# Kernel optimization log

Hardware: AMD Instinct MI355X
Metric: run time of the kernel (lower is better)

The kernel has to match this reference:

```python
import jax, jax.numpy as jnp
import numpy as np
from jax import lax

# Dense emulation of the irregular graph stage (repo helpers img2graph /
# IrregularMaxPool2d / GraphConv2d): nodes = pixels of the stride-4 grid.
# Where pooling_mask==1, a 2x2 block is max-pooled (pooled value replicated
# over the block) and subsequent GraphConv2d gathers neighbors with offset 2
# (dilation 2); where mask==0 the node keeps resolution and offset 1.


def _conv(x, w, b, dil=1):
    p = dil  # SAME padding for a 3x3 kernel with dilation `dil`
    y = lax.conv_general_dilated(x, w, (1, 1), ((p, p), (p, p)),
                                 rhs_dilation=(dil, dil),
                                 dimension_numbers=('NCHW', 'OIHW', 'NCHW'))
    return y + b[None, :, None, None]


def _maxpool2(x):
    return lax.reduce_window(x, -jnp.inf, lax.max, (1, 1, 2, 2), (1, 1, 2, 2), 'VALID')


def _up2(x):
    return jnp.repeat(jnp.repeat(x, 2, axis=2), 2, axis=3)


def setup_inputs() -> dict:
    key = jax.random.key(0)
    ks = jax.random.split(key, 12)
    B, H, W = 4, 384, 384
    inp = {
        'batch': jax.random.normal(ks[0], (B, 3, H, W), jnp.float32),
        'pooling_mask': jax.random.randint(ks[1], (B, 1, H // 8, W // 8), 0, 2, jnp.int32),
    }
    cfg = [(3, 64), (64, 64), (64, 128), (128, 128), (128, 256),
           (256, 256), (256, 256), (256, 512), (512, 512), (512, 512)]
    for i, (cin, cout) in enumerate(cfg):
        scale = float(np.sqrt(2.0 / (cin * 9)))  # He init for 3x3 conv
        inp[f'W{i+1}'] = jax.random.normal(ks[2 + (i % 10)], (cout, cin, 3, 3), jnp.float32) * scale
        inp[f'b{i+1}'] = jnp.zeros((cout,), jnp.float32)
    return inp


def reference(batch, pooling_mask, W1, b1, W2, b2, W3, b3, W4, b4, W5, b5,
              W6, b6, W7, b7, W8, b8, W9, b9, W10, b10):
    x = jax.nn.relu(_conv(batch, W1, b1))
    x = jax.nn.relu(_conv(x, W2, b2))
    x = _maxpool2(x)                                  # H/2
    x = jax.nn.relu(_conv(x, W3, b3))
    x = jax.nn.relu(_conv(x, W4, b4))
    x = _maxpool2(x)                                  # H/4 (OS4)
    x = jax.nn.relu(_conv(x, W5, b5))
    x = jax.nn.relu(_conv(x, W6, b6))
    x = jax.nn.relu(_conv(x, W7, b7))
    # img2graph + IrregularMaxPool2d (number_pools=1)
    m = (pooling_mask > 0).astype(x.dtype)            # [B,1,H/8,W/8]
    m_up = _up2(m)                                    # [B,1,H/4,W/4]
    x = m_up * _up2(_maxpool2(x)) + (1.0 - m_up) * x  # pool 2x2 where mask==1

    # GraphConv2d: per-node neighbor offset = 1 + mask (spatially varying dilation)
    def gconv(h, w, b):
        return m_up * _conv(h, w, b, dil=2) + (1.0 - m_up) * _conv(h, w, b, dil=1)

    x = jax.nn.relu(gconv(x, W8, b8))
    x = jax.nn.relu(gconv(x, W9, b9))
    x = jax.nn.relu(gconv(x, W10, b10))               # use_relu=True
    return x  # graph2img: nodes already laid out on the stride-4 grid
```

## Files before the change

### kernel.cpp

```cpp
#include <hip/hip_runtime.h>


typedef __attribute__((ext_vector_type(8))) short short8;
typedef __attribute__((ext_vector_type(4))) float f32x4;

__device__ __forceinline__ float b2f(ushort u) {
    return __uint_as_float(((unsigned)u) << 16);
}
__device__ __forceinline__ ushort f2b(float f) {
    unsigned x = __float_as_uint(f);
    x += 0x7FFFu + ((x >> 16) & 1u);
    return (ushort)(x >> 16);
}
__device__ __forceinline__ ushort bmax(ushort a, ushort b) {
    return b2f(a) > b2f(b) ? a : b;
}

__global__ __launch_bounds__(256)
void repack_w(const float* __restrict__ w, ushort* __restrict__ wp, int Cin, int Cout)
{
    int n = Cout * Cin * 9;
    int i = blockIdx.x * 256 + threadIdx.x;
    if (i >= n) return;
    int CBl = Cin / 32;
    int c   = i & 31;
    int co  = (i >> 5) % Cout;
    int cbt = i / (32 * Cout);
    int cb  = cbt % CBl;
    int t   = cbt / CBl;
    int ci  = cb * 32 + c;
    wp[i] = f2b(w[((size_t)co * Cin + ci) * 9 + t]);
}

__global__ __launch_bounds__(256)
void l1_conv(const float* __restrict__ in, const float* __restrict__ w,
             const float* __restrict__ bias, ushort* __restrict__ out)
{
    const int H = 384, W = 384;
    __shared__ float s[3][18][18];
    const int tid = threadIdx.x;
    const int tilesX = W / 16;
    const int x0 = (blockIdx.x % tilesX) * 16;
    const int y0 = (blockIdx.x / tilesX) * 16;
    const int b  = blockIdx.z;

    for (int i = tid; i < 3 * 18 * 18; i += 256) {
        int ci = i / (18 * 18);
        int r  = i % (18 * 18);
        int iy = r / 18, ix = r % 18;
        int gy = y0 - 1 + iy, gx = x0 - 1 + ix;
        float v = 0.f;
        if ((unsigned)gy < (unsigned)H && (unsigned)gx < (unsigned)W)
            v = in[((size_t)(b * 3 + ci) * H + gy) * W + gx];
        s[ci][iy][ix] = v;
    }
    __syncthreads();

    const int tx = tid & 15, ty = tid >> 4;
    float iv[3][3][3];
    #pragma unroll
    for (int ci = 0; ci < 3; ++ci)
        #pragma unroll
        for (int ky = 0; ky < 3; ++ky)
            #pragma unroll
            for (int kx = 0; kx < 3; ++kx)
                iv[ci][ky][kx] = s[ci][ty + ky][tx + kx];

    size_t pix = ((size_t)(b * H + y0 + ty) * W + x0 + tx);
    #pragma unroll
    for (int c4 = 0; c4 < 4; ++c4) {
        __align__(16) ushort ob[16];
        #pragma unroll
        for (int co = 0; co < 16; ++co) {
            int coG = c4 * 16 + co;
            float a = bias[coG];
            #pragma unroll
            for (int ci = 0; ci < 3; ++ci)
                #pragma unroll
                for (int ky = 0; ky < 3; ++ky)
                    #pragma unroll
                    for (int kx = 0; kx < 3; ++kx)
                        a = fmaf(w[((size_t)coG * 3 + ci) * 9 + ky * 3 + kx],
                                 iv[ci][ky][kx], a);
            a = a > 0.f ? a : 0.f;
            ob[co] = f2b(a);
        }
        *(short8*)&out[pix * 64 + c4 * 16]     = *(short8*)&ob[0];
        *(short8*)&out[pix * 64 + c4 * 16 + 8] = *(short8*)&ob[8];
    }
}

__global__ __launch_bounds__(256)
void maxpool_nhwc(const ushort* __restrict__ in, ushort* __restrict__ out,
                  int Ho, int Wo, int C)
{
    int n = 4 * Ho * Wo * (C / 8);
    int i = blockIdx.x * 256 + threadIdx.x;
    if (i >= n) return;
    int c8 = i % (C / 8);
    int pi = i / (C / 8);
    int x = pi % Wo, y = (pi / Wo) % Ho, b = pi / (Wo * Ho);
    int Hi = Ho * 2, Wi = Wo * 2;
    const ushort* p = in + ((size_t)(b * Hi + 2 * y) * Wi + 2 * x) * C + c8 * 8;
    short8 v00 = *(const short8*)p;
    short8 v01 = *(const short8*)(p + C);
    short8 v10 = *(const short8*)(p + (size_t)Wi * C);
    short8 v11 = *(const short8*)(p + (size_t)Wi * C + C);
    short8 o;
    #pragma unroll
    for (int j = 0; j < 8; ++j)
        o[j] = (short)bmax(bmax((ushort)v00[j], (ushort)v01[j]),
                           bmax((ushort)v10[j], (ushort)v11[j]));
    *(short8*)(out + (size_t)i * 8) = o;
}

__global__ __launch_bounds__(256)
void irpool_nhwc(const ushort* __restrict__ in, const int* __restrict__ mask,
                 ushort* __restrict__ out)
{
    const int C = 256, H = 96, Wd = 96;
    int n = 4 * H * Wd * (C / 8);
    int i = blockIdx.x * 256 + threadIdx.x;
    if (i >= n) return;
    int c8 = i % (C / 8);
    int pi = i / (C / 8);
    int x = pi % Wd, y = (pi / Wd) % H, b = pi / (Wd * H);
    int m = mask[(b * 48 + (y >> 1)) * 48 + (x >> 1)];
    short8 o;
    if (m) {
        int y0 = y & ~1, x0 = x & ~1;
        const ushort* p = in + ((size_t)(b * H + y0) * Wd + x0) * C + c8 * 8;
        short8 v00 = *(const short8*)p;
        short8 v01 = *(const short8*)(p + C);
        short8 v10 = *(const short8*)(p + (size_t)Wd * C);
        short8 v11 = *(const short8*)(p + (size_t)Wd * C + C);
        #pragma unroll
        for (int j = 0; j < 8; ++j)
            o[j] = (short)bmax(bmax((ushort)v00[j], (ushort)v01[j]),
                               bmax((ushort)v10[j], (ushort)v11[j]));
    } else {
        o = *(const short8*)(in + (size_t)pi * C + c8 * 8);
    }
    *(short8*)(out + (size_t)pi * C + c8 * 8) = o;
}

template<int TR, int BN, int CIN, int COUT, int H, int W, bool GCONV, bool FINAL>
__global__ __launch_bounds__(256)
void conv_mfma(const ushort* __restrict__ in, const ushort* __restrict__ wp,
               const float* __restrict__ bias, void* __restrict__ outv,
               const int* __restrict__ mask)
{
    constexpr int BM  = TR * 16;
    constexpr int CB  = CIN / 32;
    constexpr int HA  = GCONV ? 2 : 1;
    constexpr int CW  = 16 + 2 * HA;
    constexpr int CR  = TR + 2 * HA;
    constexpr int NCH = CR * CW;
    constexpr int WM  = BM / 64;
    constexpr int NSA = NCH * 4;
    constexpr int NSLA = (NSA + 255) / 256;
    constexpr int NSB = 3 * BN * 2;
    constexpr int NSLB = (NSB + 255) / 256;

    __shared__ __align__(16) ushort sA[NCH * 40];
    __shared__ __align__(16) ushort sB[3 * BN * 40];

    const int tid  = threadIdx.x;
    const int lane = tid & 63;
    const int wv   = tid >> 6;
    const int wm   = wv % WM;
    const int wn   = wv / WM;
    const int col  = lane & 15;
    const int quad = lane >> 4;

    const int tiles_x = W / 16, tiles_y = H / TR;
    int sp = blockIdx.x;
    const int b  = sp / (tiles_x * tiles_y);
    int rr = sp - b * tiles_x * tiles_y;
    const int ty = rr / tiles_x;
    const int tx = rr - ty * tiles_x;
    const int y0 = ty * TR, x0 = tx * 16;
    const int co0 = blockIdx.y * BN;

    int dA[4], aoff[4];
    #pragma unroll
    for (int mt = 0; mt < 4; ++mt) {
        dA[mt] = 1;
        if (GCONV) {
            int y = y0 + wm * 4 + mt, x = x0 + col;
            dA[mt] = mask[(b * (H / 2) + (y >> 1)) * (W / 2) + (x >> 1)] ? 2 : 1;
        }
        aoff[mt] = (HA + wm * 4 + mt) * CW + HA + col;
    }

    short8 pA[NSLA];
    short8 pB[NSLB][2];

    auto loadA = [&](int cb) {
        #pragma unroll
        for (int k = 0; k < NSLA; ++k) {
            int i = tid + k * 256;
            short8 v = {0, 0, 0, 0, 0, 0, 0, 0};
            if (NSA == NSLA * 256 || i < NSA) {
                int chunk = i >> 2, part = i & 3;
                int yy = chunk / CW, xx = chunk - yy * CW;
                int gy = y0 - HA + yy, gx = x0 - HA + xx;
                if ((unsigned)gy < (unsigned)H && (unsigned)gx < (unsigned)W)
                    v = *(const short8*)(in + ((size_t)(b * H + gy) * W + gx) * CIN
                                         + cb * 32 + part * 8);
            }
            pA[k] = v;
        }
    };
    auto storeA = [&]() {
        #pragma unroll
        for (int k = 0; k < NSLA; ++k) {
            int i = tid + k * 256;
            if (NSA == NSLA * 256 || i < NSA) {
                int chunk = i >> 2, part = i & 3;
                *(short8*)&sA[chunk * 40 + part * 8] = pA[k];
            }
        }
    };
    auto loadB = [&](int s) {
        int cb = s / 3, row = s % 3;
        #pragma unroll
        for (int k = 0; k < NSLB; ++k) {
            int i = tid + k * 256;
            if (NSB == NSLB * 256 || i < NSB) {
                int tl = i / (BN * 2);
                int r  = i % (BN * 2);
                int co = r >> 1, half = r & 1;
                const ushort* gp = wp
                    + ((size_t)((row * 3 + tl) * CB + cb) * COUT + co0 + co) * 32
                    + half * 16;
                pB[k][0] = *(const short8*)gp;
                pB[k][1] = *(const short8*)(gp + 8);
            }
        }
    };
    auto storeB = [&]() {
        #pragma unroll
        for (int k = 0; k < NSLB; ++k) {
            int i = tid + k * 256;
            if (NSB == NSLB * 256 || i < NSB) {
                int tl = i / (BN * 2);
                int r  = i % (BN * 2);
                int co = r >> 1, half = r & 1;
                *(short8*)&sB[(tl * BN + co) * 40 + half * 16]     = pB[k][0];
                *(short8*)&sB[(tl * BN + co) * 40 + half * 16 + 8] = pB[k][1];
            }
        }
    };

    f32x4 acc[4][4];
    #pragma unroll
    for (int i = 0; i < 4; ++i)
        #pragma unroll
        for (int j = 0; j < 4; ++j)
            acc[i][j] = (f32x4){0.f, 0.f, 0.f, 0.f};

    loadA(0);
    loadB(0);
    storeA();
    storeB();
    __syncthreads();

    for (int s = 0; s < 3 * CB; ++s) {
        const int row  = s % 3;
        const bool last = (s == 3 * CB - 1);
        if (!last) {
            loadB(s + 1);
            if (row == 2) loadA(s / 3 + 1);
        }
        const int ky = row - 1;
        #pragma unroll
        for (int j = 0; j < 3; ++j) {
            const int kx = j - 1;
            short8 af[4], bf4[4];
            #pragma unroll
            for (int i = 0; i < 4; ++i) {
                int chunk = aoff[i] + dA[i] * (ky * CW + kx);
                af[i]  = *(const short8*)&sA[chunk * 40 + quad * 8];
                bf4[i] = *(const short8*)&sB[(j * BN + wn * 64 + i * 16 + col) * 40
                                             + quad * 8];
            }
            #pragma unroll
            for (int mt = 0; mt < 4; ++mt)
                #pragma unroll
                for (int nt = 0; nt < 4; ++nt)
                    acc[mt][nt] = __builtin_amdgcn_mfma_f32_16x16x32_bf16(
                        af[mt], bf4[nt], acc[mt][nt], 0, 0, 0);
        }
        if (!last) {
            __syncthreads();
            storeB();
            if (row == 2) storeA();
            __syncthreads();
        }
    }

    if (!FINAL) {
        ushort* outp = (ushort*)outv;
        #pragma unroll
        for (int mt = 0; mt < 4; ++mt) {
            int y = y0 + wm * 4 + mt;
            #pragma unroll
            for (int nt = 0; nt < 4; ++nt) {
                int co = co0 + wn * 64 + nt * 16 + col;
                float bv = bias[co];
                #pragma unroll
                for (int r2 = 0; r2 < 4; ++r2) {
                    int x = x0 + quad * 4 + r2;
                    float vv = acc[mt][nt][r2] + bv;
                    vv = vv > 0.f ? vv : 0.f;
                    outp[((size_t)(b * H + y) * W + x) * COUT + co] = f2b(vv);
                }
            }
        }
    } else {
        float* outp = (float*)outv;
        #pragma unroll
        for (int mt = 0; mt < 4; ++mt) {
            int y = y0 + wm * 4 + mt;
            #pragma unroll
            for (int nt = 0; nt < 4; ++nt) {
                int co = co0 + wn * 64 + nt * 16 + col;
                float bv = bias[co];
                f32x4 vv;
                #pragma unroll
                for (int r2 = 0; r2 < 4; ++r2) {
                    float z = acc[mt][nt][r2] + bv;
                    vv[r2] = z > 0.f ? z : 0.f;
                }
                *(f32x4*)&outp[((size_t)(b * COUT + co) * H + y) * W + x0 + quad * 4] = vv;
            }
        }
    }
}

extern "C" void kernel_launch(void* const* d_in, const int* in_sizes, int n_in,
                              void* d_out, int out_size, void* d_ws, size_t ws_size,
                              hipStream_t stream)
{
    const float* x    = (const float*)d_in[0];
    const int*   mask = (const int*)d_in[1];
    const float* Wt[10];
    const float* bs[10];
    for (int i = 0; i < 10; ++i) {
        Wt[i] = (const float*)d_in[2 + 2 * i];
        bs[i] = (const float*)d_in[3 + 2 * i];
    }

    const size_t ACT = (size_t)4 * 384 * 384 * 64;
    ushort* A  = (ushort*)d_ws;
    ushort* Bb = A + ACT;
    ushort* wpbase = Bb + ACT;

    static const int cins[10]  = {3, 64, 64, 128, 128, 256, 256, 256, 512, 512};
    static const int couts[10] = {64, 64, 128, 128, 256, 256, 256, 512, 512, 512};
    ushort* wp[10];
    size_t wo = 0;
    for (int l = 1; l < 10; ++l) {
        wp[l] = wpbase + wo;
        wo += (size_t)couts[l] * cins[l] * 9;
    }
    for (int l = 1; l < 10; ++l) {
        int n = couts[l] * cins[l] * 9;
        repack_w<<<(n + 255) / 256, 256, 0, stream>>>(Wt[l], wp[l], cins[l], couts[l]);
    }

    l1_conv<<<dim3(24 * 24, 1, 4), 256, 0, stream>>>(x, Wt[0], bs[0], A);

    conv_mfma<16, 64, 64, 64, 384, 384, false, false>
        <<<dim3(4 * 24 * 24, 1), 256, 0, stream>>>(A, wp[1], bs[1], Bb, nullptr);
    maxpool_nhwc<<<(4 * 192 * 192 * 8 + 255) / 256, 256, 0, stream>>>(Bb, A, 192, 192, 64);

    conv_mfma<8, 128, 64, 128, 192, 192, false, false>
        <<<dim3(4 * 24 * 12, 1), 256, 0, stream>>>(A, wp[2], bs[2], Bb, nullptr);
    conv_mfma<8, 128, 128, 128, 192, 192, false, false>
        <<<dim3(4 * 24 * 12, 1), 256, 0, stream>>>(Bb, wp[3], bs[3], A, nullptr);
    maxpool_nhwc<<<(4 * 96 * 96 * 16 + 255) / 256, 256, 0, stream>>>(A, Bb, 96, 96, 128);

    conv_mfma<8, 128, 128, 256, 96, 96, false, false>
        <<<dim3(4 * 12 * 6, 2), 256, 0, stream>>>(Bb, wp[4], bs[4], A, nullptr);
    conv_mfma<8, 128, 256, 256, 96, 96, false, false>
        <<<dim3(4 * 12 * 6, 2), 256, 0, stream>>>(A, wp[5], bs[5], Bb, nullptr);
    conv_mfma<8, 128, 256, 256, 96, 96, false, false>
        <<<dim3(4 * 12 * 6, 2), 256, 0, stream>>>(Bb, wp[6], bs[6], A, nullptr);

    irpool_nhwc<<<(4 * 96 * 96 * 32 + 255) / 256, 256, 0, stream>>>(A, mask, Bb);

    conv_mfma<8, 128, 256, 512, 96, 96, true, false>
        <<<dim3(4 * 12 * 6, 4), 256, 0, stream>>>(Bb, wp[7], bs[7], A, mask);
    conv_mfma<8, 128, 512, 512, 96, 96, true, false>
        <<<dim3(4 * 12 * 6, 4), 256, 0, stream>>>(A, wp[8], bs[8], Bb, mask);
    conv_mfma<8, 128, 512, 512, 96, 96, true, true>
        <<<dim3(4 * 12 * 6, 4), 256, 0, stream>>>(Bb, wp[9], bs[9], d_out, mask);

    (void)in_sizes; (void)n_in; (void)out_size; (void)ws_size;
}
```

Before: 972.1 us.

## Reorganize LDS and packed weight layout into quad-major 8-channel planes

The weight repack now stores each 32-channel block as four 8-channel quads laid out contiguously across output channels. B staging becomes a single 16-byte load per slot with contiguous LDS stores. The A tile in LDS also moves from a padded 40-element row stride to quad-major planes (with a small plane padding). The aim is to remove LDS bank conflicts in the MFMA fragment reads and to simplify global and LDS addressing. A static_assert now requires 12*BN to be a multiple of 256.

```diff
diff --git a/kernel.cpp b/kernel.cpp
--- a/kernel.cpp
+++ b/kernel.cpp
@@ -23,12 +23,14 @@
     int i = blockIdx.x * 256 + threadIdx.x;
     if (i >= n) return;
     int CBl = Cin / 32;
-    int c   = i & 31;
-    int co  = (i >> 5) % Cout;
-    int cbt = i / (32 * Cout);
-    int cb  = cbt % CBl;
-    int t   = cbt / CBl;
-    int ci  = cb * 32 + c;
+    int c8   = i & 7;
+    int co   = (i >> 3) % Cout;
+    int rest = (i >> 3) / Cout;
+    int q    = rest & 3;
+    int cbt  = rest >> 2;
+    int cb   = cbt % CBl;
+    int t    = cbt / CBl;
+    int ci   = cb * 32 + q * 8 + c8;
     wp[i] = f2b(w[((size_t)co * Cin + ci) * 9 + t]);
 }
 
@@ -150,20 +152,22 @@
                const float* __restrict__ bias, void* __restrict__ outv,
                const int* __restrict__ mask)
 {
-    constexpr int BM  = TR * 16;
-    constexpr int CB  = CIN / 32;
-    constexpr int HA  = GCONV ? 2 : 1;
-    constexpr int CW  = 16 + 2 * HA;
-    constexpr int CR  = TR + 2 * HA;
-    constexpr int NCH = CR * CW;
-    constexpr int WM  = BM / 64;
-    constexpr int NSA = NCH * 4;
+    constexpr int BM   = TR * 16;
+    constexpr int CB   = CIN / 32;
+    constexpr int HA   = GCONV ? 2 : 1;
+    constexpr int CW   = 16 + 2 * HA;
+    constexpr int CR   = TR + 2 * HA;
+    constexpr int NCH  = CR * CW;
+    constexpr int NCHP = NCH + 2;
+    constexpr int WM   = BM / 64;
+    constexpr int NSA  = NCH * 4;
     constexpr int NSLA = (NSA + 255) / 256;
-    constexpr int NSB = 3 * BN * 2;
-    constexpr int NSLB = (NSB + 255) / 256;
-
-    __shared__ __align__(16) ushort sA[NCH * 40];
-    __shared__ __align__(16) ushort sB[3 * BN * 40];
+    constexpr int NSB  = 12 * BN;
+    constexpr int NSLB = NSB / 256;
+    static_assert(NSB % 256 == 0, "B staging must tile 256 threads");
+
+    __shared__ __align__(16) ushort sA[4 * NCHP * 8];
+    __shared__ __align__(16) ushort sB[12 * BN * 8];
 
     const int tid  = threadIdx.x;
     const int lane = tid & 63;
@@ -194,7 +198,7 @@
     }
 
     short8 pA[NSLA];
-    short8 pB[NSLB][2];
+    short8 pB[NSLB];
 
     auto loadA = [&](int cb) {
         #pragma unroll
@@ -218,7 +222,7 @@
             int i = tid + k * 256;
             if (NSA == NSLA * 256 || i < NSA) {
                 int chunk = i >> 2, part = i & 3;
-                *(short8*)&sA[chunk * 40 + part * 8] = pA[k];
+                *(short8*)&sA[(part * NCHP + chunk) * 8] = pA[k];
             }
         }
     };
@@ -227,29 +231,20 @@
         #pragma unroll
         for (int k = 0; k < NSLB; ++k) {
             int i = tid + k * 256;
-            if (NSB == NSLB * 256 || i < NSB) {
-                int tl = i / (BN * 2);
-                int r  = i % (BN * 2);
-                int co = r >> 1, half = r & 1;
-                const ushort* gp = wp
-                    + ((size_t)((row * 3 + tl) * CB + cb) * COUT + co0 + co) * 32
-                    + half * 16;
-                pB[k][0] = *(const short8*)gp;
-                pB[k][1] = *(const short8*)(gp + 8);
-            }
+            int co = i % BN;
+            int rq = i / BN;
+            const ushort* gp = wp
+                + (((size_t)(row * 3 + (rq >> 2)) * CB + cb) * 4 + (rq & 3))
+                      * COUT * 8
+                + (size_t)(co0 + co) * 8;
+            pB[k] = *(const short8*)gp;
         }
     };
     auto storeB = [&]() {
         #pragma unroll
         for (int k = 0; k < NSLB; ++k) {
             int i = tid + k * 256;
-            if (NSB == NSLB * 256 || i < NSB) {
-                int tl = i / (BN * 2);
-                int r  = i % (BN * 2);
-                int co = r >> 1, half = r & 1;
-                *(short8*)&sB[(tl * BN + co) * 40 + half * 16]     = pB[k][0];
-                *(short8*)&sB[(tl * BN + co) * 40 + half * 16 + 8] = pB[k][1];
-            }
+            *(short8*)&sB[(size_t)i * 8] = pB[k];
         }
     };
 
@@ -281,9 +276,9 @@
             #pragma unroll
             for (int i = 0; i < 4; ++i) {
                 int chunk = aoff[i] + dA[i] * (ky * CW + kx);
-                af[i]  = *(const short8*)&sA[chunk * 40 + quad * 8];
-                bf4[i] = *(const short8*)&sB[(j * BN + wn * 64 + i * 16 + col) * 40
-                                             + quad * 8];
+                af[i]  = *(const short8*)&sA[(quad * NCHP + chunk) * 8];
+                bf4[i] = *(const short8*)&sB[((j * 4 + quad) * BN
+                                              + wn * 64 + i * 16 + col) * 8];
             }
             #pragma unroll
             for (int mt = 0; mt < 4; ++mt)
```

Result: no change. 957.3 us (-1.5%).
